# Performance work log

Measured on AMD Instinct MI355X. Metric: run time of the kernel, lower is better.

## Reference

```python
import math
import jax, jax.numpy as jnp
import numpy as np
from jax import lax

B, C, H, W = 4, 256, 64, 64
TD = 256
GROUPS = 32
EPS = 1e-5


def group_norm(x, scale, bias, groups=GROUPS, eps=EPS):
    b, c, h, w = x.shape
    xg = x.reshape(b, groups, c // groups, h, w)
    m = xg.mean(axis=(2, 3, 4), keepdims=True)
    v = xg.var(axis=(2, 3, 4), keepdims=True)
    xn = ((xg - m) * lax.rsqrt(v + eps)).reshape(b, c, h, w)
    return xn * scale[None, :, None, None] + bias[None, :, None, None]


def conv3x3(x, w, b):
    y = lax.conv_general_dilated(x, w, (1, 1), 'SAME',
                                 dimension_numbers=('NCHW', 'OIHW', 'NCHW'))
    return y + b[None, :, None, None]


def setup_inputs() -> dict:
    key = jax.random.key(0)
    ks = jax.random.split(key, 10)
    s = 0.02
    return {
        'x': jax.random.normal(ks[0], (B, C, H, W), jnp.float32),
        'time_embed': jax.random.normal(ks[1], (B, TD), jnp.float32),
        # ResNetBlock params
        'gn1_s': jnp.ones((C,), jnp.float32), 'gn1_b': jnp.zeros((C,), jnp.float32),
        'conv1_w': jax.random.normal(ks[2], (C, C, 3, 3), jnp.float32) * s,
        'conv1_b': jnp.zeros((C,), jnp.float32),
        'mlp_w': jax.random.normal(ks[3], (2 * C, TD), jnp.float32) * s,
        'mlp_b': jnp.zeros((2 * C,), jnp.float32),
        'gn2_s': jnp.ones((C,), jnp.float32), 'gn2_b': jnp.zeros((C,), jnp.float32),
        'conv2_w': jax.random.normal(ks[4], (C, C, 3, 3), jnp.float32) * s,
        'conv2_b': jnp.zeros((C,), jnp.float32),
        # SelfAttention params (n_head=1, 1x1 convs stored as matrices)
        'gnA_s': jnp.ones((C,), jnp.float32), 'gnA_b': jnp.zeros((C,), jnp.float32),
        'qkv_w': jax.random.normal(ks[5], (3 * C, C), jnp.float32) * s,
        'out_w': jax.random.normal(ks[6], (C, C), jnp.float32) * s,
        'out_b': jnp.zeros((C,), jnp.float32),
    }


def reference(x, time_embed, gn1_s, gn1_b, conv1_w, conv1_b, mlp_w, mlp_b,
              gn2_s, gn2_b, conv2_w, conv2_b, gnA_s, gnA_b, qkv_w, out_w, out_b):
    # --- ResNetBlock ---
    h = conv3x3(jax.nn.silu(group_norm(x, gn1_s, gn1_b)), conv1_w, conv1_b)
    # time-embedding FiLM: SiLU -> Linear -> (gamma, beta)
    gb = jnp.dot(jax.nn.silu(time_embed), mlp_w.T) + mlp_b  # [B, 2C]
    gamma, beta = jnp.split(gb[:, :, None, None], 2, axis=1)
    h = (1.0 + gamma) * h + beta
    h = conv3x3(jax.nn.silu(group_norm(h, gn2_s, gn2_b)), conv2_w, conv2_b)
    xr = h + x  # res_conv is Identity since dim == dim_out

    # --- SelfAttention (n_head=1, scale = sqrt(channel)) ---
    b, c, hh, ww = xr.shape
    n = group_norm(xr, gnA_s, gnA_b)
    qkv = jnp.einsum('oc,bchw->bohw', qkv_w, n)  # [B, 3C, H, W]
    q, k, v = jnp.split(qkv.reshape(b, 3 * c, hh * ww), 3, axis=1)  # [B,C,HW] each
    attn = jnp.einsum('bcs,bct->bst', q, k) / math.sqrt(c)  # [B, HW, HW]
    attn = jax.nn.softmax(attn, axis=-1)
    o = jnp.einsum('bst,bct->bcs', attn, v).reshape(b, c, hh, ww)
    o = jnp.einsum('oc,bchw->bohw', out_w, o) + out_b[None, :, None, None]
    return o + xr
```

## Files before the change

kernel.cpp:

```cpp
#include <hip/hip_runtime.h>
#include <math.h>

#define SS 4096
#define NE 4194304

typedef __attribute__((ext_vector_type(8))) short short8;
typedef __attribute__((ext_vector_type(4))) short short4v;
typedef __attribute__((ext_vector_type(4))) float f32x4;
typedef __attribute__((ext_vector_type(16))) float f32x16;

__device__ __forceinline__ float wave_sum(float v) {
#pragma unroll
  for (int off = 32; off > 0; off >>= 1) v += __shfl_xor(v, off, 64);
  return v;
}
__device__ __forceinline__ float silu_f(float y) { return y / (1.f + __expf(-y)); }

__device__ __forceinline__ unsigned short to_bf(float x) {
  union { float f; unsigned u; } v; v.f = x;
  unsigned r = v.u + 0x7FFFu + ((v.u >> 16) & 1u);
  return (unsigned short)(r >> 16);
}
__device__ __forceinline__ float bf2f(short s) {
  union { unsigned u; float f; } v;
  v.u = ((unsigned)(unsigned short)s) << 16;
  return v.f;
}

__global__ __launch_bounds__(256) void gn_stats_k(const float* __restrict__ x,
                                                  float* __restrict__ stats) {
  const float4* p = (const float4*)(x + (size_t)blockIdx.x * 32768);
  float s = 0.f, q = 0.f;
  for (int i = threadIdx.x; i < 8192; i += 256) {
    float4 v = p[i];
    s += v.x + v.y + v.z + v.w;
    q += v.x * v.x + v.y * v.y + v.z * v.z + v.w * v.w;
  }
  s = wave_sum(s); q = wave_sum(q);
  __shared__ float red[8];
  int wid = threadIdx.x >> 6;
  if ((threadIdx.x & 63) == 0) { red[wid] = s; red[wid + 4] = q; }
  __syncthreads();
  if (threadIdx.x == 0) {
    s = red[0] + red[1] + red[2] + red[3];
    q = red[4] + red[5] + red[6] + red[7];
    float m = s * (1.f / 32768.f);
    float var = q * (1.f / 32768.f) - m * m;
    stats[blockIdx.x * 2] = m;
    stats[blockIdx.x * 2 + 1] = rsqrtf(var + 1e-5f);
  }
}

template <int DO_SILU>
__global__ __launch_bounds__(256) void gn_t_k(const float* __restrict__ x,
    const float* __restrict__ stats, const float* __restrict__ sc,
    const float* __restrict__ bi, short* __restrict__ G) {
  __shared__ short T[64][72];
  const int tid = threadIdx.x;
  const int st = blockIdx.x & 63;
  const int ct = (blockIdx.x >> 6) & 3;
  const int b = blockIdx.x >> 8;
  const int s0 = st * 64, c0 = ct * 64;
#pragma unroll
  for (int r = 0; r < 4; ++r) {
    int idx = r * 256 + tid;
    int c_l = idx >> 4, s4 = idx & 15;
    int c = c0 + c_l;
    int sidx = (b * 32 + (c >> 3)) * 2;
    float m = stats[sidx], rs = stats[sidx + 1];
    float a = sc[c] * rs;
    float t = bi[c] - m * a;
    float4 v = *(const float4*)(x + ((size_t)(b * 256 + c)) * 4096 + s0 + s4 * 4);
    float o0 = v.x * a + t, o1 = v.y * a + t, o2 = v.z * a + t, o3 = v.w * a + t;
    if (DO_SILU) { o0 = silu_f(o0); o1 = silu_f(o1); o2 = silu_f(o2); o3 = silu_f(o3); }
    T[s4 * 4 + 0][c_l] = (short)to_bf(o0);
    T[s4 * 4 + 1][c_l] = (short)to_bf(o1);
    T[s4 * 4 + 2][c_l] = (short)to_bf(o2);
    T[s4 * 4 + 3][c_l] = (short)to_bf(o3);
  }
  __syncthreads();
#pragma unroll
  for (int r = 0; r < 2; ++r) {
    int idx = r * 256 + tid;
    int s_l = idx >> 3, cg = idx & 7;
    *(short8*)(G + ((size_t)(b * 4096 + s0 + s_l)) * 256 + c0 + cg * 8) =
        *(const short8*)&T[s_l][cg * 8];
  }
}

__global__ __launch_bounds__(256) void prep_k(
    const float* __restrict__ conv1_w, const float* __restrict__ conv2_w,
    const float* __restrict__ qkv_w, const float* __restrict__ out_w,
    const float* __restrict__ te, const float* __restrict__ mlp_w,
    const float* __restrict__ mlp_b, short* __restrict__ Wt1,
    short* __restrict__ Wt2, short* __restrict__ wqb, short* __restrict__ wob,
    float* __restrict__ gbuf) {
  const int bid = blockIdx.x, tid = threadIdx.x;
  if (bid < 512) {
    __shared__ short L[9][256];
    const float* w = (bid < 256) ? conv1_w : conv2_w;
    short* wt = (bid < 256) ? Wt1 : Wt2;
    const int oc = bid & 255;
    const float* wp = w + (size_t)oc * 2304;
    for (int i = tid; i < 2304; i += 256) {
      int ic = i / 9, t = i - ic * 9;
      L[t][ic] = (short)to_bf(wp[i]);
    }
    __syncthreads();
    for (int i = tid; i < 2304; i += 256) {
      int t = i >> 8, ic = i & 255;
      wt[((size_t)(t * 256 + oc)) * 256 + ic] = L[t][ic];
    }
  } else if (bid < 1280) {
    int row = bid - 512;
    float sc = (row < 256) ? 0.0625f : 1.f;
    wqb[(size_t)row * 256 + tid] = (short)to_bf(qkv_w[(size_t)row * 256 + tid] * sc);
  } else if (bid < 1536) {
    int row = bid - 1280;
    wob[(size_t)row * 256 + tid] = (short)to_bf(out_w[(size_t)row * 256 + tid]);
  } else {
    int t2 = (bid - 1536) * 256 + tid;
    int b = t2 >> 9, jj = t2 & 511;
    const float* tp = te + b * 256;
    const float* wp = mlp_w + jj * 256;
    float acc = mlp_b[jj];
    for (int t = 0; t < 256; ++t) acc += silu_f(tp[t]) * wp[t];
    gbuf[t2] = acc;
  }
}

__device__ __forceinline__ short8 ld2x4(const short* p) {
  short4v lo = *(const short4v*)p;
  short4v hi = *(const short4v*)(p + 4);
  short8 r;
  r[0] = lo[0]; r[1] = lo[1]; r[2] = lo[2]; r[3] = lo[3];
  r[4] = hi[0]; r[5] = hi[1]; r[6] = hi[2]; r[7] = hi[3];
  return r;
}

template <int MODE>
__global__ __launch_bounds__(256, 1) void conv_mfma_k(
    const short* __restrict__ G, const short* __restrict__ Wt,
    const float* __restrict__ bias, const float* __restrict__ gb,
    const float* __restrict__ resid, float* __restrict__ out) {
  __shared__ __align__(16) short Xs[6][66][36];
  __shared__ __align__(16) short Ws[9][32][32];
  const int tid = threadIdx.x;
  const int oc0 = (blockIdx.x & 7) * 32;
  const int oy = ((blockIdx.x >> 3) & 15) * 4;
  const int b = blockIdx.x >> 7;
  const int wv = tid >> 6, lane = tid & 63;
  const int ln = lane & 31, hf = lane >> 5;

  f32x16 O0 = {}, O1 = {};

  for (int ic0 = 0; ic0 < 256; ic0 += 32) {
    __syncthreads();
    for (int i = tid; i < 1584; i += 256) {
      int r = i / 264;
      int rem = i - r * 264;
      int col = rem >> 2, g = rem & 3;
      int gy = oy + r - 1, gx = col - 1;
      short4v lo = {0, 0, 0, 0}, hi = {0, 0, 0, 0};
      if ((unsigned)gy < 64u && (unsigned)gx < 64u) {
        const short* gp = G + ((size_t)(b * 4096 + gy * 64 + gx)) * 256 + ic0 + g * 8;
        lo = *(const short4v*)gp;
        hi = *(const short4v*)(gp + 4);
      }
      *(short4v*)&Xs[r][col][g * 8] = lo;
      *(short4v*)&Xs[r][col][g * 8 + 4] = hi;
    }
    for (int i = tid; i < 1152; i += 256) {
      int t = i >> 7;
      int rem = i & 127;
      int o = rem >> 2, g = rem & 3;
      *(short8*)&Ws[t][o][g * 8] =
          *(const short8*)(Wt + ((size_t)(t * 256 + oc0 + o)) * 256 + ic0 + g * 8);
    }
    __syncthreads();
    for (int t = 0; t < 9; ++t) {
      const int dy = t / 3, dx = t - dy * 3;
      const short* xrow = &Xs[wv + dy][0][0];
#pragma unroll
      for (int ks = 0; ks < 2; ++ks) {
        short8 a0 = *(const short8*)&Ws[t][ln][ks * 16 + hf * 8];
        short8 b0 = ld2x4(xrow + (ln + dx) * 36 + ks * 16 + hf * 8);
        short8 b1 = ld2x4(xrow + (32 + ln + dx) * 36 + ks * 16 + hf * 8);
        O0 = __builtin_amdgcn_mfma_f32_32x32x16_bf16(a0, b0, O0, 0, 0, 0);
        O1 = __builtin_amdgcn_mfma_f32_32x32x16_bf16(a0, b1, O1, 0, 0, 0);
      }
    }
  }
  const int srow = (oy + wv) * 64;
#pragma unroll
  for (int i = 0; i < 16; ++i) {
    int oc = oc0 + (i & 3) + 8 * (i >> 2) + 4 * hf;
    float bi = bias[oc];
    size_t base = ((size_t)(b * 256 + oc)) * 4096 + srow;
    float v0 = O0[i] + bi, v1 = O1[i] + bi;
    if (MODE == 0) {
      float ga = 1.f + gb[b * 512 + oc], be = gb[b * 512 + 256 + oc];
      v0 = ga * v0 + be;
      v1 = ga * v1 + be;
    } else {
      v0 += resid[base + ln];
      v1 += resid[base + 32 + ln];
    }
    out[base + ln] = v0;
    out[base + 32 + ln] = v1;
  }
}

template <int MODE>
__global__ __launch_bounds__(256, 2) void gemm1x1_k(
    const short* __restrict__ X, const short* __restrict__ W,
    const float* __restrict__ bias, const float* __restrict__ ml,
    short* __restrict__ q, short* __restrict__ k, short* __restrict__ v,
    float* __restrict__ out) {
  __shared__ __align__(16) short sh[18432];
  const int tid = threadIdx.x;
  const int o0 = blockIdx.x * 64;
  const int s0 = blockIdx.y * 256;
  const int b = blockIdx.z;
  const int w = tid >> 6, lane = tid & 63, ln = lane & 31, hf = lane >> 5;
  {
    const int o = tid >> 2, g = tid & 3;
#pragma unroll
    for (int j = 0; j < 8; ++j) {
      int c = (g * 8 + j) * 8;
      *(short8*)&sh[o * 264 + c] = *(const short8*)(W + (size_t)(o0 + o) * 256 + c);
    }
  }
  __syncthreads();
  f32x16 acc[2][2] = {{{}, {}}, {{}, {}}};
  if (MODE == 0) {
    const short* xp = X + ((size_t)(b * 4096 + s0 + w * 64)) * 256;
    short8 bf0 = *(const short8*)(xp + (size_t)ln * 256 + hf * 8);
    short8 bf1 = *(const short8*)(xp + (size_t)(32 + ln) * 256 + hf * 8);
#pragma unroll
    for (int ks = 0; ks < 16; ++ks) {
      short8 a0 = *(const short8*)&sh[ln * 264 + ks * 16 + hf * 8];
      short8 a1 = *(const short8*)&sh[(32 + ln) * 264 + ks * 16 + hf * 8];
      short8 nb0 = bf0, nb1 = bf1;
      if (ks < 15) {
        nb0 = *(const short8*)(xp + (size_t)ln * 256 + (ks + 1) * 16 + hf * 8);
        nb1 = *(const short8*)(xp + (size_t)(32 + ln) * 256 + (ks + 1) * 16 + hf * 8);
      }
      acc[0][0] = __builtin_amdgcn_mfma_f32_32x32x16_bf16(a0, bf0, acc[0][0], 0, 0, 0);
      acc[0][1] = __builtin_amdgcn_mfma_f32_32x32x16_bf16(a0, bf1, acc[0][1], 0, 0, 0);
      acc[1][0] = __builtin_amdgcn_mfma_f32_32x32x16_bf16(a1, bf0, acc[1][0], 0, 0, 0);
      acc[1][1] = __builtin_amdgcn_mfma_f32_32x32x16_bf16(a1, bf1, acc[1][1], 0, 0, 0);
      bf0 = nb0; bf1 = nb1;
    }
  } else {
    const size_t r0 = (size_t)b * 4096 + s0 + w * 64 + ln;
    const size_t r1 = r0 + 32;
    float inv0 = 1.f / (ml[r0] + ml[16384 + r0] + ml[32768 + r0] + ml[49152 + r0]);
    float inv1 = 1.f / (ml[r1] + ml[16384 + r1] + ml[32768 + r1] + ml[49152 + r1]);
#pragma unroll 4
    for (int ks = 0; ks < 16; ++ks) {
      float t0[8] = {0, 0, 0, 0, 0, 0, 0, 0}, t1[8] = {0, 0, 0, 0, 0, 0, 0, 0};
#pragma unroll
      for (int z = 0; z < 4; ++z) {
        short8 p0 = *(const short8*)(X + ((size_t)z * 16384 + r0) * 256 + ks * 16 + hf * 8);
        short8 p1 = *(const short8*)(X + ((size_t)z * 16384 + r1) * 256 + ks * 16 + hf * 8);
#pragma unroll
        for (int jj = 0; jj < 8; ++jj) { t0[jj] += bf2f(p0[jj]); t1[jj] += bf2f(p1[jj]); }
      }
      short8 bf0, bf1;
#pragma unroll
      for (int jj = 0; jj < 8; ++jj) {
        bf0[jj] = (short)to_bf(t0[jj] * inv0);
        bf1[jj] = (short)to_bf(t1[jj] * inv1);
      }
      short8 a0 = *(const short8*)&sh[ln * 264 + ks * 16 + hf * 8];
      short8 a1 = *(const short8*)&sh[(32 + ln) * 264 + ks * 16 + hf * 8];
      acc[0][0] = __builtin_amdgcn_mfma_f32_32x32x16_bf16(a0, bf0, acc[0][0], 0, 0, 0);
      acc[0][1] = __builtin_amdgcn_mfma_f32_32x32x16_bf16(a0, bf1, acc[0][1], 0, 0, 0);
      acc[1][0] = __builtin_amdgcn_mfma_f32_32x32x16_bf16(a1, bf0, acc[1][0], 0, 0, 0);
      acc[1][1] = __builtin_amdgcn_mfma_f32_32x32x16_bf16(a1, bf1, acc[1][1], 0, 0, 0);
    }
  }
  if (MODE == 1) {
#pragma unroll
    for (int os = 0; os < 2; ++os)
#pragma unroll
      for (int ss = 0; ss < 2; ++ss)
#pragma unroll
        for (int i = 0; i < 16; ++i) {
          int oc = o0 + os * 32 + (i & 3) + 8 * (i >> 2) + 4 * hf;
          size_t idx = ((size_t)(b * 256 + oc)) * 4096 + s0 + w * 64 + ss * 32 + ln;
          out[idx] = out[idx] + acc[os][ss][i] + bias[oc];
        }
  } else if (o0 >= 512) {
#pragma unroll
    for (int os = 0; os < 2; ++os)
#pragma unroll
      for (int ss = 0; ss < 2; ++ss)
#pragma unroll
        for (int i = 0; i < 16; ++i) {
          int oc = (o0 - 512) + os * 32 + (i & 3) + 8 * (i >> 2) + 4 * hf;
          v[((size_t)(b * 256 + oc)) * 4096 + s0 + w * 64 + ss * 32 + ln] =
              (short)to_bf(acc[os][ss][i]);
        }
  } else {
    __syncthreads();
#pragma unroll
    for (int os = 0; os < 2; ++os)
#pragma unroll
      for (int ss = 0; ss < 2; ++ss)
#pragma unroll
        for (int i = 0; i < 16; ++i) {
          int o_l = os * 32 + (i & 3) + 8 * (i >> 2) + 4 * hf;
          int s_l = ss * 32 + ln;
          sh[(w * 64 + s_l) * 72 + o_l] = (short)to_bf(acc[os][ss][i]);
        }
    __syncthreads();
    short* dst = (o0 < 256) ? q : k;
    const int co = (o0 < 256) ? o0 : o0 - 256;
    const short* src = &sh[(w * 64 + lane) * 72];
    short* gp = dst + ((size_t)(b * 4096 + s0 + w * 64 + lane)) * 256 + co;
#pragma unroll
    for (int j = 0; j < 8; ++j)
      *(short8*)(gp + j * 8) = *(const short8*)(src + j * 8);
  }
}

__global__ __launch_bounds__(256, 2) void attn_k(const short* __restrict__ qb,
    const short* __restrict__ kb, const short* __restrict__ vb,
    short* __restrict__ part, float* __restrict__ ml) {
  __shared__ __align__(16) short qls[64 * 268];
  __shared__ __align__(16) short vls[256 * 68];
  __shared__ __align__(16) short pls[64 * 68];
  __shared__ __align__(16) float lss[64 * 4];
  const int tid = threadIdx.x;
  const int j = blockIdx.x & 7;
  const int b = j >> 1;
  const int idx = ((blockIdx.x >> 3) << 1) | (j & 1);
  const int z = idx >> 6;
  const int s0 = (idx & 63) * 64;
  const int kv0 = z * 1024;
  const int w = tid >> 6, lane = tid & 63, ln = lane & 15, qd = lane >> 4;

  {
    const short* qsrc = qb + ((size_t)(b * 4096 + s0)) * 256;
    for (int i = tid; i < 2048; i += 256) {
      int r = i >> 5, cc = i & 31;
      *(short8*)&qls[r * 268 + cc * 8] = *(const short8*)(qsrc + (size_t)r * 256 + cc * 8);
    }
  }
  const f32x4 z4 = {0.f, 0.f, 0.f, 0.f};
  f32x4 O[4][4];
#pragma unroll
  for (int g = 0; g < 4; ++g)
#pragma unroll
    for (int cs = 0; cs < 4; ++cs) O[g][cs] = z4;
  float l_loc[4] = {0.f, 0.f, 0.f, 0.f};

  const short* kbb = kb + ((size_t)(b * 4096 + kv0)) * 256;
  const short* vbb = vb + ((size_t)b * 256) * 4096 + kv0;

  const int vr = tid >> 3;
  const int vc = (tid & 7) * 8;

  short8 kreg[8], vreg[8];
#pragma unroll
  for (int ks = 0; ks < 8; ++ks)
    kreg[ks] = *(const short8*)(kbb + ((size_t)(w * 16 + ln)) * 256 + ks * 32 + qd * 8);
#pragma unroll
  for (int p = 0; p < 8; ++p)
    vreg[p] = *(const short8*)(vbb + ((size_t)(vr + p * 32)) * 4096 + vc);
  __syncthreads();

  for (int t0 = 0; t0 < 1024; t0 += 64) {
    const int tn = (t0 + 64 < 1024) ? t0 + 64 : t0;
#pragma unroll
    for (int p = 0; p < 8; ++p)
      *(short8*)&vls[(vr + p * 32) * 68 + vc] = vreg[p];
#pragma unroll
    for (int p = 0; p < 8; ++p)
      vreg[p] = *(const short8*)(vbb + ((size_t)(vr + p * 32)) * 4096 + tn + vc);
    f32x4 S[4] = {z4, z4, z4, z4};
#pragma unroll
    for (int ks = 0; ks < 8; ++ks) {
#pragma unroll
      for (int g = 0; g < 4; ++g) {
        short8 qf = *(const short8*)&qls[(g * 16 + ln) * 268 + ks * 32 + qd * 8];
        S[g] = __builtin_amdgcn_mfma_f32_16x16x32_bf16(kreg[ks], qf, S[g], 0, 0, 0);
      }
    }
#pragma unroll
    for (int ks = 0; ks < 8; ++ks)
      kreg[ks] = *(const short8*)(kbb + ((size_t)(tn + w * 16 + ln)) * 256 + ks * 32 + qd * 8);
#pragma unroll
    for (int g = 0; g < 4; ++g) {
      const int q = g * 16 + ln;
      float p0 = __expf(S[g][0]), p1 = __expf(S[g][1]);
      float p2 = __expf(S[g][2]), p3 = __expf(S[g][3]);
      unsigned lo = (unsigned)to_bf(p0) | ((unsigned)to_bf(p1) << 16);
      unsigned hi = (unsigned)to_bf(p2) | ((unsigned)to_bf(p3) << 16);
      *(unsigned*)&pls[q * 68 + w * 16 + qd * 4] = lo;
      *(unsigned*)&pls[q * 68 + w * 16 + qd * 4 + 2] = hi;
      l_loc[g] += (p0 + p1) + (p2 + p3);
    }
    __syncthreads();
#pragma unroll
    for (int kc = 0; kc < 2; ++kc) {
      short8 pf[4];
#pragma unroll
      for (int g = 0; g < 4; ++g)
        pf[g] = *(const short8*)&pls[(g * 16 + ln) * 68 + kc * 32 + qd * 8];
#pragma unroll
      for (int cs = 0; cs < 4; ++cs) {
        short8 vf = *(const short8*)&vls[(w * 64 + cs * 16 + ln) * 68 + kc * 32 + qd * 8];
#pragma unroll
        for (int g = 0; g < 4; ++g)
          O[g][cs] = __builtin_amdgcn_mfma_f32_16x16x32_bf16(vf, pf[g], O[g][cs], 0, 0, 0);
      }
    }
    __syncthreads();
  }
#pragma unroll
  for (int g = 0; g < 4; ++g) {
    float lg = l_loc[g];
    lg += __shfl_xor(lg, 16, 64);
    lg += __shfl_xor(lg, 32, 64);
    if (qd == 0) lss[(g * 16 + ln) * 4 + w] = lg;
  }
  __syncthreads();
  const size_t prow = (size_t)z * 16384 + (size_t)b * 4096 + s0;
#pragma unroll
  for (int g = 0; g < 4; ++g) {
    short* pp = part + (prow + g * 16 + ln) * 256 + w * 64 + qd * 4;
#pragma unroll
    for (int cs = 0; cs < 4; ++cs) {
      short4v o4;
      o4[0] = (short)to_bf(O[g][cs][0]);
      o4[1] = (short)to_bf(O[g][cs][1]);
      o4[2] = (short)to_bf(O[g][cs][2]);
      o4[3] = (short)to_bf(O[g][cs][3]);
      *(short4v*)(pp + cs * 16) = o4;
    }
  }
  if (w == 0 && qd == 0) {
#pragma unroll
    for (int g = 0; g < 4; ++g) {
      const int q = g * 16 + ln;
      f32x4 lt = *(const f32x4*)&lss[q * 4];
      ml[(size_t)z * 16384 + (size_t)b * 4096 + s0 + q] =
          (lt[0] + lt[1]) + (lt[2] + lt[3]);
    }
  }
}

extern "C" void kernel_launch(void* const* d_in, const int* in_sizes, int n_in,
                              void* d_out, int out_size, void* d_ws, size_t ws_size,
                              hipStream_t stream) {
  const float* x       = (const float*)d_in[0];
  const float* te      = (const float*)d_in[1];
  const float* gn1_s   = (const float*)d_in[2];
  const float* gn1_b   = (const float*)d_in[3];
  const float* conv1_w = (const float*)d_in[4];
  const float* conv1_b = (const float*)d_in[5];
  const float* mlp_w   = (const float*)d_in[6];
  const float* mlp_b   = (const float*)d_in[7];
  const float* gn2_s   = (const float*)d_in[8];
  const float* gn2_b   = (const float*)d_in[9];
  const float* conv2_w = (const float*)d_in[10];
  const float* conv2_b = (const float*)d_in[11];
  const float* gnA_s   = (const float*)d_in[12];
  const float* gnA_b   = (const float*)d_in[13];
  const float* qkv_w   = (const float*)d_in[14];
  const float* out_w   = (const float*)d_in[15];
  const float* out_b   = (const float*)d_in[16];
  float* out = (float*)d_out;

  float* bufA  = (float*)d_ws;
  float* bufB  = bufA + NE;
  short* qb    = (short*)(bufB + NE);
  short* kb    = qb + NE;
  short* vb    = kb + NE;
  float* mlb   = (float*)(vb + NE);
  float* stats = mlb + 65536;
  float* gbuf  = stats + 768;
  short* wqb   = (short*)(gbuf + 2048);
  short* wob   = wqb + 196608;
  short* G     = qb;
  short* Wt1   = kb;
  short* Wt2   = Wt1 + 589824;
  short* nT    = (short*)bufA;
  short* partb = (short*)bufA;

  prep_k<<<1544, 256, 0, stream>>>(conv1_w, conv2_w, qkv_w, out_w, te, mlp_w,
                                   mlp_b, Wt1, Wt2, wqb, wob, gbuf);
  gn_stats_k<<<128, 256, 0, stream>>>(x, stats);
  gn_t_k<1><<<1024, 256, 0, stream>>>(x, stats, gn1_s, gn1_b, G);
  conv_mfma_k<0><<<512, 256, 0, stream>>>(G, Wt1, conv1_b, gbuf, nullptr, bufB);
  gn_stats_k<<<128, 256, 0, stream>>>(bufB, stats + 256);
  gn_t_k<1><<<1024, 256, 0, stream>>>(bufB, stats + 256, gn2_s, gn2_b, G);
  conv_mfma_k<1><<<512, 256, 0, stream>>>(G, Wt2, conv2_b, nullptr, x, out);
  gn_stats_k<<<128, 256, 0, stream>>>(out, stats + 512);
  gn_t_k<0><<<1024, 256, 0, stream>>>(out, stats + 512, gnA_s, gnA_b, nT);
  gemm1x1_k<0><<<dim3(12, 16, 4), 256, 0, stream>>>(nT, wqb, nullptr, nullptr,
                                                    qb, kb, vb, nullptr);
  attn_k<<<1024, 256, 0, stream>>>(qb, kb, vb, partb, mlb);
  gemm1x1_k<1><<<dim3(4, 16, 4), 256, 0, stream>>>(partb, wob, out_b, mlb,
                                                   nullptr, nullptr, nullptr, out);
}
```

Baseline: 408.3 us.

## Fuse group-norm statistics into conv epilogues and prep kernel

Removes the three standalone group-norm statistics kernels. The first GN's sums are computed by extra blocks in the prep kernel. The second and third GN's sums and sums of squares are accumulated in the conv epilogues with wave reductions and atomicAdd. The consuming gn_t kernels now derive mean and rsqrt from the raw sums. This saves two full 16 MB re-reads and three launches, in exchange for atomics and nondeterministic float summation order.

```diff
diff --git a/kernel.cpp b/kernel.cpp
--- a/kernel.cpp
+++ b/kernel.cpp
@@ -25,30 +25,6 @@
   union { unsigned u; float f; } v;
   v.u = ((unsigned)(unsigned short)s) << 16;
   return v.f;
-}
-
-__global__ __launch_bounds__(256) void gn_stats_k(const float* __restrict__ x,
-                                                  float* __restrict__ stats) {
-  const float4* p = (const float4*)(x + (size_t)blockIdx.x * 32768);
-  float s = 0.f, q = 0.f;
-  for (int i = threadIdx.x; i < 8192; i += 256) {
-    float4 v = p[i];
-    s += v.x + v.y + v.z + v.w;
-    q += v.x * v.x + v.y * v.y + v.z * v.z + v.w * v.w;
-  }
-  s = wave_sum(s); q = wave_sum(q);
-  __shared__ float red[8];
-  int wid = threadIdx.x >> 6;
-  if ((threadIdx.x & 63) == 0) { red[wid] = s; red[wid + 4] = q; }
-  __syncthreads();
-  if (threadIdx.x == 0) {
-    s = red[0] + red[1] + red[2] + red[3];
-    q = red[4] + red[5] + red[6] + red[7];
-    float m = s * (1.f / 32768.f);
-    float var = q * (1.f / 32768.f) - m * m;
-    stats[blockIdx.x * 2] = m;
-    stats[blockIdx.x * 2 + 1] = rsqrtf(var + 1e-5f);
-  }
 }
 
 template <int DO_SILU>
@@ -67,7 +43,10 @@
     int c_l = idx >> 4, s4 = idx & 15;
     int c = c0 + c_l;
     int sidx = (b * 32 + (c >> 3)) * 2;
-    float m = stats[sidx], rs = stats[sidx + 1];
+    float ssum = stats[sidx], qsum = stats[sidx + 1];
+    float m = ssum * (1.f / 32768.f);
+    float var = qsum * (1.f / 32768.f) - m * m;
+    float rs = rsqrtf(var + 1e-5f);
     float a = sc[c] * rs;
     float t = bi[c] - m * a;
     float4 v = *(const float4*)(x + ((size_t)(b * 256 + c)) * 4096 + s0 + s4 * 4);
@@ -92,9 +71,10 @@
     const float* __restrict__ conv1_w, const float* __restrict__ conv2_w,
     const float* __restrict__ qkv_w, const float* __restrict__ out_w,
     const float* __restrict__ te, const float* __restrict__ mlp_w,
-    const float* __restrict__ mlp_b, short* __restrict__ Wt1,
-    short* __restrict__ Wt2, short* __restrict__ wqb, short* __restrict__ wob,
-    float* __restrict__ gbuf) {
+    const float* __restrict__ mlp_b, const float* __restrict__ x,
+    short* __restrict__ Wt1, short* __restrict__ Wt2, short* __restrict__ wqb,
+    short* __restrict__ wob, float* __restrict__ gbuf,
+    float* __restrict__ stats) {
   const int bid = blockIdx.x, tid = threadIdx.x;
   if (bid < 512) {
     __shared__ short L[9][256];
@@ -118,7 +98,7 @@
   } else if (bid < 1536) {
     int row = bid - 1280;
     wob[(size_t)row * 256 + tid] = (short)to_bf(out_w[(size_t)row * 256 + tid]);
-  } else {
+  } else if (bid < 1544) {
     int t2 = (bid - 1536) * 256 + tid;
     int b = t2 >> 9, jj = t2 & 511;
     const float* tp = te + b * 256;
@@ -126,6 +106,27 @@
     float acc = mlp_b[jj];
     for (int t = 0; t < 256; ++t) acc += silu_f(tp[t]) * wp[t];
     gbuf[t2] = acc;
+  } else if (bid < 1672) {
+    const int sub = bid - 1544;
+    const float4* p = (const float4*)(x + (size_t)sub * 32768);
+    float s = 0.f, q = 0.f;
+    for (int i = tid; i < 8192; i += 256) {
+      float4 v = p[i];
+      s += v.x + v.y + v.z + v.w;
+      q += v.x * v.x + v.y * v.y + v.z * v.z + v.w * v.w;
+    }
+    s = wave_sum(s); q = wave_sum(q);
+    __shared__ float red[8];
+    int wid = tid >> 6;
+    if ((tid & 63) == 0) { red[wid] = s; red[wid + 4] = q; }
+    __syncthreads();
+    if (tid == 0) {
+      stats[sub * 2] = red[0] + red[1] + red[2] + red[3];
+      stats[sub * 2 + 1] = red[4] + red[5] + red[6] + red[7];
+    }
+  } else {
+    stats[256 + tid] = 0.f;
+    stats[512 + tid] = 0.f;
   }
 }
 
@@ -142,7 +143,8 @@
 __global__ __launch_bounds__(256, 1) void conv_mfma_k(
     const short* __restrict__ G, const short* __restrict__ Wt,
     const float* __restrict__ bias, const float* __restrict__ gb,
-    const float* __restrict__ resid, float* __restrict__ out) {
+    const float* __restrict__ resid, float* __restrict__ out,
+    float* __restrict__ sraw) {
   __shared__ __align__(16) short Xs[6][66][36];
   __shared__ __align__(16) short Ws[9][32][32];
   const int tid = threadIdx.x;
@@ -192,6 +194,7 @@
     }
   }
   const int srow = (oy + wv) * 64;
+  float gs[4] = {0.f, 0.f, 0.f, 0.f}, gq[4] = {0.f, 0.f, 0.f, 0.f};
 #pragma unroll
   for (int i = 0; i < 16; ++i) {
     int oc = oc0 + (i & 3) + 8 * (i >> 2) + 4 * hf;
@@ -208,6 +211,19 @@
     }
     out[base + ln] = v0;
     out[base + 32 + ln] = v1;
+    int jg = i >> 2;
+    gs[jg] += v0 + v1;
+    gq[jg] += v0 * v0 + v1 * v1;
+  }
+#pragma unroll
+  for (int jg = 0; jg < 4; ++jg) {
+    float s = wave_sum(gs[jg]);
+    float q = wave_sum(gq[jg]);
+    if (lane == 0) {
+      int gidx = (b * 32 + (oc0 >> 3) + jg) * 2;
+      atomicAdd(&sraw[gidx], s);
+      atomicAdd(&sraw[gidx + 1], q);
+    }
   }
 }
 
@@ -491,15 +507,14 @@
   short* nT    = (short*)bufA;
   short* partb = (short*)bufA;
 
-  prep_k<<<1544, 256, 0, stream>>>(conv1_w, conv2_w, qkv_w, out_w, te, mlp_w,
-                                   mlp_b, Wt1, Wt2, wqb, wob, gbuf);
-  gn_stats_k<<<128, 256, 0, stream>>>(x, stats);
+  prep_k<<<1673, 256, 0, stream>>>(conv1_w, conv2_w, qkv_w, out_w, te, mlp_w,
+                                   mlp_b, x, Wt1, Wt2, wqb, wob, gbuf, stats);
   gn_t_k<1><<<1024, 256, 0, stream>>>(x, stats, gn1_s, gn1_b, G);
-  conv_mfma_k<0><<<512, 256, 0, stream>>>(G, Wt1, conv1_b, gbuf, nullptr, bufB);
-  gn_stats_k<<<128, 256, 0, stream>>>(bufB, stats + 256);
+  conv_mfma_k<0><<<512, 256, 0, stream>>>(G, Wt1, conv1_b, gbuf, nullptr, bufB,
+                                          stats + 256);
   gn_t_k<1><<<1024, 256, 0, stream>>>(bufB, stats + 256, gn2_s, gn2_b, G);
-  conv_mfma_k<1><<<512, 256, 0, stream>>>(G, Wt2, conv2_b, nullptr, x, out);
-  gn_stats_k<<<128, 256, 0, stream>>>(out, stats + 512);
+  conv_mfma_k<1><<<512, 256, 0, stream>>>(G, Wt2, conv2_b, nullptr, x, out,
+                                          stats + 512);
   gn_t_k<0><<<1024, 256, 0, stream>>>(out, stats + 512, gnA_s, gnA_b, nT);
   gemm1x1_k<0><<<dim3(12, 16, 4), 256, 0, stream>>>(nT, wqb, nullptr, nullptr,
                                                     qb, kb, vb, nullptr);
```

New measurement: 428.1 us. 1.05x slower.
